# Kernel optimization log

Measured on AMD Instinct MI355X. Metric: run time of the kernel, lower is better.

## Reference

```python
import jax, jax.numpy as jnp
import numpy as np

N_NODES = 100000
N_EDGES = 1600000
N_GRAPHS = 64
IN_DIM, HID, OUT_DIM = 64, 128, 32


def _glorot(key, shape):
    lim = float(np.sqrt(6.0 / (shape[0] + shape[1])))
    return jax.random.uniform(key, shape, jnp.float32, -lim, lim)


def setup_inputs() -> dict:
    key = jax.random.key(0)
    ks = jax.random.split(key, 20)
    x = jax.random.normal(ks[0], (N_NODES, IN_DIM), jnp.float32)
    edge_index = jax.random.randint(ks[1], (2, N_EDGES), 0, N_NODES, jnp.int64)
    batch = jnp.sort(jax.random.randint(ks[2], (N_NODES,), 0, N_GRAPHS, jnp.int64))
    d = {"x": x, "edge_index": edge_index, "batch": batch}
    dims = [(IN_DIM, HID), (HID, HID), (HID, HID), (HID, HID), (HID, OUT_DIM)]
    names = ["W1", "W2", "W3", "W4", "Wo"]
    bnames = ["b1", "b2", "b3", "b4", "bo"]
    for i, ((di, do), wn, bn) in enumerate(zip(dims, names, bnames)):
        d[wn] = _glorot(ks[3 + i], (di, do))
        d[bn] = jnp.zeros((do,), jnp.float32)
    # MLP: 32 -> 64 -> 8 -> 8  (hidden_dim//2, output_dim//2, output_dim//4)
    mdims = [(OUT_DIM, HID // 2), (HID // 2, OUT_DIM // 2), (OUT_DIM // 2, OUT_DIM // 4)]
    for i, (di, do) in enumerate(mdims):
        d[f"M{i+1}w"] = _glorot(ks[10 + i], (di, do))
        d[f"M{i+1}b"] = jnp.zeros((do,), jnp.float32)
    return d


def _gcn(x, src, dst, norm, W, b, n):
    h = x @ W                                    # [N, d_out] dense GEMM
    msg = h[src] * norm[:, None]                 # gather + normalize
    agg = jax.ops.segment_sum(msg, dst, num_segments=n)  # scatter-add
    return agg + b


def reference(x, edge_index, batch, W1, b1, W2, b2, W3, b3, W4, b4, Wo, bo,
              M1w, M1b, M2w, M2b, M3w, M3b):
    n = x.shape[0]
    # add self loops (PyG GCNConv default)
    loops = jnp.arange(n, dtype=edge_index.dtype)
    src = jnp.concatenate([edge_index[0], loops])
    dst = jnp.concatenate([edge_index[1], loops])
    # symmetric degree normalization: D^{-1/2} (A+I) D^{-1/2}
    deg = jax.ops.segment_sum(jnp.ones_like(src, dtype=x.dtype), dst, num_segments=n)
    dinv = jnp.where(deg > 0, jax.lax.rsqrt(deg), 0.0)
    norm = dinv[src] * dinv[dst]                 # [E+N]

    h = jax.nn.relu(_gcn(x, src, dst, norm, W1, b1, n))
    for W, b in ((W2, b2), (W3, b3), (W4, b4)):
        h = jax.nn.relu(_gcn(h, src, dst, norm, W, b, n))
    h = _gcn(h, src, dst, norm, Wo, bo, n)       # [N, 32]

    # global mean pool over graphs
    sums = jax.ops.segment_sum(h, batch, num_segments=N_GRAPHS)
    cnts = jax.ops.segment_sum(jnp.ones((n,), h.dtype), batch, num_segments=N_GRAPHS)
    g = sums / jnp.maximum(cnts, 1.0)[:, None]   # [G, 32]

    g = jax.nn.relu(g @ M1w + M1b)
    g = jax.nn.relu(g @ M2w + M2b)
    return g @ M3w + M3b                          # [G, 8]
```

## Files before the change

kernel.cpp:

```cpp
#include <hip/hip_runtime.h>


static constexpr int TPB = 256;
static constexpr int NBKT = 128;
static constexpr int NCHK = 256;

using f32x4  = __attribute__((ext_vector_type(4))) float;
using bf16x8 = __attribute__((ext_vector_type(8))) short;

__device__ __forceinline__ float u2f(unsigned u) { return __uint_as_float(u); }

__device__ __forceinline__ unsigned short bf1(float a) {
    unsigned u = __float_as_uint(a);
    u += 0x7FFFu + ((u >> 16) & 1u);
    return (unsigned short)(u >> 16);
}

__device__ __forceinline__ unsigned bf2(float a, float b) {
    unsigned ua = __float_as_uint(a);
    unsigned ub = __float_as_uint(b);
    ua += 0x7FFFu + ((ua >> 16) & 1u);
    ub += 0x7FFFu + ((ub >> 16) & 1u);
    return (ua >> 16) | (ub & 0xFFFF0000u);
}

__global__ __launch_bounds__(256) void k_hist(const int* __restrict__ dst,
                                              int* __restrict__ histT, int E, int CS) {
    __shared__ int h[NBKT];
    int c = blockIdx.x, t = threadIdx.x;
    if (t < NBKT) h[t] = 0;
    __syncthreads();
    int e0 = c * CS, e1 = min(e0 + CS, E);
    for (int e = e0 + t; e < e1; e += 256)
        atomicAdd(&h[dst[e] >> 10], 1);
    __syncthreads();
    if (t < NBKT) histT[t * NCHK + c] = h[t];
}

__global__ __launch_bounds__(256) void k_scanS(const int* __restrict__ histT,
                                               int* __restrict__ stg) {
    constexpr int TOT = NBKT * NCHK;
    constexpr int PER = TOT / 256;
    __shared__ int s[256];
    int t = threadIdx.x;
    int base = t * PER;
    int sum = 0;
    for (int i = 0; i < PER; ++i) sum += histT[base + i];
    s[t] = sum;
    __syncthreads();
    for (int off = 1; off < 256; off <<= 1) {
        int add = (t >= off) ? s[t - off] : 0;
        __syncthreads();
        s[t] += add;
        __syncthreads();
    }
    int run = (t > 0) ? s[t - 1] : 0;
    for (int i = 0; i < PER; ++i) {
        stg[base + i] = run;
        run += histT[base + i];
    }
}

__global__ __launch_bounds__(256) void k_bucket(const int* __restrict__ src,
                                                const int* __restrict__ dst,
                                                const int* __restrict__ stg,
                                                unsigned* __restrict__ staging,
                                                int E, int CS) {
    __shared__ int cur[NBKT];
    int c = blockIdx.x, t = threadIdx.x;
    if (t < NBKT) cur[t] = stg[t * NCHK + c];
    __syncthreads();
    int e0 = c * CS, e1 = min(e0 + CS, E);
    for (int e = e0 + t; e < e1; e += 256) {
        int d = dst[e];
        int p = atomicAdd(&cur[d >> 10], 1);
        staging[p] = ((unsigned)src[e] << 10) | (unsigned)(d & 1023);
    }
}

__global__ __launch_bounds__(256) void k_deg(const unsigned* __restrict__ staging,
                                             const int* __restrict__ stg,
                                             int* __restrict__ cnt, int E, int n) {
    __shared__ int deg[1024];
    int r = blockIdx.x, t = threadIdx.x;
    for (int i = t; i < 1024; i += 256) deg[i] = 0;
    __syncthreads();
    int s0 = stg[r * NCHK];
    int s1 = (r == NBKT - 1) ? E : stg[(r + 1) * NCHK];
    for (int e = s0 + t; e < s1; e += 256)
        atomicAdd(&deg[staging[e] & 1023u], 1);
    __syncthreads();
    int b = r << 10;
    for (int i = t; i < 1024; i += 256)
        if (b + i < n) cnt[b + i] = deg[i];
}

__global__ void k_scanA(const int* __restrict__ cnt, int* __restrict__ rowptr,
                        int* __restrict__ bsum, int n) {
    __shared__ int s[TPB];
    int t = threadIdx.x;
    int i = blockIdx.x * TPB + t;
    s[t] = (i < n) ? cnt[i] : 0;
    __syncthreads();
    for (int off = 1; off < TPB; off <<= 1) {
        int add = (t >= off) ? s[t - off] : 0;
        __syncthreads();
        s[t] += add;
        __syncthreads();
    }
    if (i < n) rowptr[i + 1] = s[t];
    if (t == TPB - 1) bsum[blockIdx.x] = s[t];
}

__global__ void k_scanB(const int* __restrict__ bsum, int* __restrict__ bscan, int nb) {
    __shared__ int s[512];
    int t = threadIdx.x;
    s[t] = (t < nb) ? bsum[t] : 0;
    __syncthreads();
    for (int off = 1; off < 512; off <<= 1) {
        int add = (t >= off) ? s[t - off] : 0;
        __syncthreads();
        s[t] += add;
        __syncthreads();
    }
    if (t < nb) bscan[t] = (t > 0) ? s[t - 1] : 0;
}

__global__ void k_scanC(int* __restrict__ rowptr, const int* __restrict__ bscan,
                        const int* __restrict__ cnt, float* __restrict__ dinv, int n) {
    int i = blockIdx.x * blockDim.x + threadIdx.x;
    if (i >= n) return;
    rowptr[i + 1] += bscan[i >> 8];
    dinv[i] = rsqrtf((float)cnt[i] + 1.0f);
    if (i == 0) rowptr[0] = 0;
}

__global__ __launch_bounds__(256) void k_fill2(const unsigned* __restrict__ staging,
                                               const int* __restrict__ stg,
                                               const int* __restrict__ rowptr,
                                               int* __restrict__ csr, int E, int n) {
    __shared__ int cur[1024];
    int r = blockIdx.x, t = threadIdx.x;
    int b = r << 10;
    for (int i = t; i < 1024; i += 256)
        cur[i] = (b + i < n) ? rowptr[b + i] : 0;
    __syncthreads();
    int s0 = stg[r * NCHK];
    int s1 = (r == NBKT - 1) ? E : stg[(r + 1) * NCHK];
    for (int e = s0 + t; e < s1; e += 256) {
        unsigned sd = staging[e];
        int p = atomicAdd(&cur[sd & 1023u], 1);
        csr[p] = (int)(sd >> 10);
    }
}

__global__ void k_castx(const float* __restrict__ x, const float* __restrict__ dinv,
                        unsigned short* __restrict__ xs, int n) {
    int gid = blockIdx.x * blockDim.x + threadIdx.x;
    if (gid >= n * 8) return;
    int row = gid >> 3;
    float d = dinv[row];
    const float4* xp = (const float4*)x + (size_t)gid * 2;
    float4 a = xp[0], b = xp[1];
    uint4 o;
    o.x = bf2(a.x * d, a.y * d);
    o.y = bf2(a.z * d, a.w * d);
    o.z = bf2(b.x * d, b.y * d);
    o.w = bf2(b.z * d, b.w * d);
    ((uint4*)xs)[gid] = o;
}

__global__ void k_prepw(const float* __restrict__ W1, const float* __restrict__ W2,
                        const float* __restrict__ W3, const float* __restrict__ W4,
                        const float* __restrict__ Wo,
                        unsigned short* __restrict__ wt1, unsigned short* __restrict__ wt2,
                        unsigned short* __restrict__ wt3, unsigned short* __restrict__ wt4,
                        unsigned short* __restrict__ wto) {
    int b = blockIdx.x, k = threadIdx.x;
    const float* W; unsigned short* wt; int K, OUT, nn;
    if (b < 128)      { W = W1; wt = wt1; K = 64;  OUT = 128; nn = b; }
    else if (b < 256) { W = W2; wt = wt2; K = 128; OUT = 128; nn = b - 128; }
    else if (b < 384) { W = W3; wt = wt3; K = 128; OUT = 128; nn = b - 256; }
    else if (b < 512) { W = W4; wt = wt4; K = 128; OUT = 128; nn = b - 384; }
    else              { W = Wo; wt = wto; K = 128; OUT = 32;  nn = b - 512; }
    if (nn >= OUT || k >= K) return;
    float v = W[(size_t)k * OUT + nn];
    unsigned short hi = bf1(v);
    float fhi = u2f((unsigned)hi << 16);
    unsigned short lo = bf1(v - fhi);
    wt[nn * K + k] = hi;
    wt[OUT * K + nn * K + k] = lo;
}

template <int K, int OUT, int EPI>
__global__ __launch_bounds__(256) void k_gemm_mfma(
    const unsigned short* __restrict__ Ain,
    const unsigned short* __restrict__ WT,
    const float* __restrict__ dinv,
    const float* __restrict__ bias,
    unsigned short* __restrict__ out, int n) {
    constexpr int NT = OUT / 16;
    constexpr int KT = K / 32;
    constexpr int CH = K / 8;
    __shared__ __align__(16) unsigned short Wl[2 * OUT * K];

    int t = threadIdx.x;
    {
        const uint4* wg = (const uint4*)WT;
        uint4* wl = (uint4*)Wl;
        for (int i = t; i < 2 * OUT * CH; i += 256) {
            int m = i / (OUT * CH);
            int r = i - m * (OUT * CH);
            int nn = r / CH, g = r - nn * CH;
            wl[m * OUT * CH + nn * CH + (g ^ (nn & 7))] = wg[i];
        }
    }

    int wid = t >> 6, lane = t & 63;
    int lr = lane & 15, lg = lane >> 4;
    int mbase = blockIdx.x * 128 + wid * 32;

    bf16x8 a[2][KT];
#pragma unroll
    for (int mt = 0; mt < 2; ++mt) {
        int row = mbase + mt * 16 + lr;
        row = row < n ? row : n - 1;
        const bf16x8* ap = (const bf16x8*)(Ain + (size_t)row * K);
#pragma unroll
        for (int kt = 0; kt < KT; ++kt)
            a[mt][kt] = ap[kt * 4 + lg];
    }

    __syncthreads();

    f32x4 acc[2][NT] = {};
#pragma unroll
    for (int nt = 0; nt < NT; ++nt) {
        int nn = nt * 16 + lr;
        int swz = nn & 7;
        int rowoff = nn * K;
#pragma unroll
        for (int kt = 0; kt < KT; ++kt) {
            int g = kt * 4 + lg;
            int off = rowoff + ((g ^ swz) * 8);
            bf16x8 bhi = *(const bf16x8*)&Wl[off];
            bf16x8 blo = *(const bf16x8*)&Wl[OUT * K + off];
#pragma unroll
            for (int mt = 0; mt < 2; ++mt) {
                acc[mt][nt] = __builtin_amdgcn_mfma_f32_16x16x32_bf16(
                    a[mt][kt], bhi, acc[mt][nt], 0, 0, 0);
                acc[mt][nt] = __builtin_amdgcn_mfma_f32_16x16x32_bf16(
                    a[mt][kt], blo, acc[mt][nt], 0, 0, 0);
            }
        }
    }

#pragma unroll
    for (int mt = 0; mt < 2; ++mt) {
        int rbase = mbase + mt * 16 + lg * 4;
        float dv[4];
        if (EPI == 0) {
#pragma unroll
            for (int r = 0; r < 4; ++r)
                dv[r] = (rbase + r < n) ? dinv[rbase + r] : 0.f;
        }
#pragma unroll
        for (int nt = 0; nt < NT; ++nt) {
            int col = nt * 16 + lr;
            float bb = (EPI == 1) ? bias[col] : 0.f;
#pragma unroll
            for (int r = 0; r < 4; ++r) {
                int row = rbase + r;
                if (row < n) {
                    float v = acc[mt][nt][r];
                    if (EPI == 0) v *= dv[r];
                    else v = fmaxf(v + bb, 0.f);
                    out[(size_t)row * OUT + col] = bf1(v);
                }
            }
        }
    }
}

__device__ __forceinline__ void addbf(float* acc, uint4 w) {
    acc[0] += u2f(w.x << 16); acc[1] += u2f(w.x & 0xFFFF0000u);
    acc[2] += u2f(w.y << 16); acc[3] += u2f(w.y & 0xFFFF0000u);
    acc[4] += u2f(w.z << 16); acc[5] += u2f(w.z & 0xFFFF0000u);
    acc[6] += u2f(w.w << 16); acc[7] += u2f(w.w & 0xFFFF0000u);
}

template <int D, bool RELU, bool HASBIAS, bool OUTBF>
__global__ __launch_bounds__(256) void k_gather_bf(const unsigned short* __restrict__ hsb,
                                                   const int* __restrict__ rowptr,
                                                   const int* __restrict__ csr,
                                                   const float* __restrict__ dinv,
                                                   const float* __restrict__ bias,
                                                   void* __restrict__ outp, int n) {
    constexpr int TPN = D / 8;
    int gid = blockIdx.x * blockDim.x + threadIdx.x;
    int node = gid / TPN;
    if (node >= n) return;
    int c = gid % TPN;
    const uint4* hb = (const uint4*)hsb;

    float acc[8];
    {
        uint4 v = hb[(size_t)node * TPN + c];
        acc[0] = u2f(v.x << 16); acc[1] = u2f(v.x & 0xFFFF0000u);
        acc[2] = u2f(v.y << 16); acc[3] = u2f(v.y & 0xFFFF0000u);
        acc[4] = u2f(v.z << 16); acc[5] = u2f(v.z & 0xFFFF0000u);
        acc[6] = u2f(v.w << 16); acc[7] = u2f(v.w & 0xFFFF0000u);
    }
    int j0 = rowptr[node], j1 = rowptr[node + 1];
    int j = j0;
    for (; j + 3 < j1; j += 4) {
        int s0 = csr[j], s1 = csr[j + 1], s2 = csr[j + 2], s3 = csr[j + 3];
        uint4 w0 = hb[(size_t)s0 * TPN + c];
        uint4 w1 = hb[(size_t)s1 * TPN + c];
        uint4 w2 = hb[(size_t)s2 * TPN + c];
        uint4 w3 = hb[(size_t)s3 * TPN + c];
        addbf(acc, w0); addbf(acc, w1); addbf(acc, w2); addbf(acc, w3);
    }
    for (; j < j1; ++j) {
        uint4 w0 = hb[(size_t)csr[j] * TPN + c];
        addbf(acc, w0);
    }

    float di = dinv[node];
    float r[8];
    if (HASBIAS) {
        float4 b0 = *(const float4*)&bias[c * 8];
        float4 b1 = *(const float4*)&bias[c * 8 + 4];
        r[0] = di * acc[0] + b0.x; r[1] = di * acc[1] + b0.y;
        r[2] = di * acc[2] + b0.z; r[3] = di * acc[3] + b0.w;
        r[4] = di * acc[4] + b1.x; r[5] = di * acc[5] + b1.y;
        r[6] = di * acc[6] + b1.z; r[7] = di * acc[7] + b1.w;
    } else {
#pragma unroll
        for (int i = 0; i < 8; ++i) r[i] = di * acc[i];
    }
    if (RELU) {
#pragma unroll
        for (int i = 0; i < 8; ++i) r[i] = fmaxf(r[i], 0.f);
    }
    if (OUTBF) {
        uint4 o;
        o.x = bf2(r[0], r[1]); o.y = bf2(r[2], r[3]);
        o.z = bf2(r[4], r[5]); o.w = bf2(r[6], r[7]);
        ((uint4*)outp)[(size_t)node * TPN + c] = o;
    } else {
        float4 o0 = {r[0], r[1], r[2], r[3]};
        float4 o1 = {r[4], r[5], r[6], r[7]};
        float4* op = (float4*)outp + (size_t)node * TPN * 2 + c * 2;
        op[0] = o0;
        op[1] = o1;
    }
}

__global__ __launch_bounds__(256) void k_pool(const float* __restrict__ h,
                                              const int* __restrict__ batch,
                                              float* __restrict__ g, int n) {
    __shared__ int se[2];
    __shared__ float red[8][32];
    int gi = blockIdx.x;
    int t = threadIdx.x;
    if (t == 0) {
        int lo = 0, hi = n;
        while (lo < hi) { int m = (lo + hi) >> 1; if (batch[m] < gi) lo = m + 1; else hi = m; }
        se[0] = lo;
        lo = 0; hi = n;
        while (lo < hi) { int m = (lo + hi) >> 1; if (batch[m] < gi + 1) lo = m + 1; else hi = m; }
        se[1] = lo;
    }
    __syncthreads();
    int start = se[0], end = se[1];
    int col = t & 31, sub = t >> 5;
    float acc = 0.f;
    for (int i = start + sub; i < end; i += 8)
        acc += h[(size_t)i * 32 + col];
    red[sub][col] = acc;
    __syncthreads();
    if (t < 32) {
        float s = 0.f;
#pragma unroll
        for (int q = 0; q < 8; ++q) s += red[q][t];
        float c = (float)(end - start);
        g[gi * 32 + t] = s / fmaxf(c, 1.0f);
    }
}

template <int K, int O, bool RELU>
__global__ void k_mlp(const float* __restrict__ in, const float* __restrict__ W,
                      const float* __restrict__ b, float* __restrict__ out, int G) {
    int gid = blockIdx.x * blockDim.x + threadIdx.x;
    if (gid >= G * O) return;
    int g = gid / O, j = gid % O;
    float s = b[j];
    for (int k = 0; k < K; ++k) s += in[g * K + k] * W[k * O + j];
    if (RELU) s = fmaxf(s, 0.f);
    out[gid] = s;
}

extern "C" void kernel_launch(void* const* d_in, const int* in_sizes, int n_in,
                              void* d_out, int out_size, void* d_ws, size_t ws_size,
                              hipStream_t stream) {
    const float* x    = (const float*)d_in[0];
    const int*   ei   = (const int*)d_in[1];
    const int*   batch= (const int*)d_in[2];
    const float* W1 = (const float*)d_in[3];  const float* b1 = (const float*)d_in[4];
    const float* W2 = (const float*)d_in[5];  const float* b2 = (const float*)d_in[6];
    const float* W3 = (const float*)d_in[7];  const float* b3 = (const float*)d_in[8];
    const float* W4 = (const float*)d_in[9];  const float* b4 = (const float*)d_in[10];
    const float* Wo = (const float*)d_in[11]; const float* bo = (const float*)d_in[12];
    const float* M1w = (const float*)d_in[13]; const float* M1b = (const float*)d_in[14];
    const float* M2w = (const float*)d_in[15]; const float* M2b = (const float*)d_in[16];
    const float* M3w = (const float*)d_in[17]; const float* M3b = (const float*)d_in[18];

    const int N = in_sizes[0] / 64;
    const int E = in_sizes[1] / 2;
    const int G = out_size / 8;
    const int* src  = ei;
    const int* dstp = ei + E;

    char* w = (char*)d_ws;
    unsigned short* buf1 = (unsigned short*)w; w += (size_t)N * 128 * 2;
    unsigned short* buf2 = (unsigned short*)w; w += (size_t)N * 128 * 2;
    unsigned short* hsb  = (unsigned short*)w; w += (size_t)N * 128 * 2;
    int*      csr     = (int*)w;      w += (size_t)E * 4;
    unsigned* staging = (unsigned*)w; w += (size_t)E * 4;
    int*      histT   = (int*)w;      w += NBKT * NCHK * 4;
    int*      stg     = (int*)w;      w += NBKT * NCHK * 4;
    int*      cnt     = (int*)w;      w += (size_t)N * 4;
    int*      rowptr  = (int*)w;      w += (size_t)(N + 4) * 4;
    int*      bsum    = (int*)w;      w += 4096;
    int*      bscan   = (int*)w;      w += 4096;
    float*    dinv    = (float*)w;    w += (size_t)N * 4;
    unsigned short* wt1 = (unsigned short*)w; w += 2 * 128 * 64 * 2;
    unsigned short* wt2 = (unsigned short*)w; w += 2 * 128 * 128 * 2;
    unsigned short* wt3 = (unsigned short*)w; w += 2 * 128 * 128 * 2;
    unsigned short* wt4 = (unsigned short*)w; w += 2 * 128 * 128 * 2;
    unsigned short* wto = (unsigned short*)w; w += 2 * 32 * 128 * 2;
    float*    gp      = (float*)w;    w += 64 * 32 * 4;
    float*    m1      = (float*)w;    w += 64 * 64 * 4;
    float*    m2      = (float*)w;    w += 64 * 16 * 4;

    const int NB = (N + TPB - 1) / TPB;
    const int CS = (E + NCHK - 1) / NCHK;
    const int GB = (N + 127) / 128;

    k_hist<<<NCHK, 256, 0, stream>>>(dstp, histT, E, CS);
    k_prepw<<<544, 128, 0, stream>>>(W1, W2, W3, W4, Wo, wt1, wt2, wt3, wt4, wto);
    k_scanS<<<1, 256, 0, stream>>>(histT, stg);
    k_bucket<<<NCHK, 256, 0, stream>>>(src, dstp, stg, staging, E, CS);
    k_deg<<<NBKT, 256, 0, stream>>>(staging, stg, cnt, E, N);
    k_scanA<<<NB, TPB, 0, stream>>>(cnt, rowptr, bsum, N);
    k_scanB<<<1, 512, 0, stream>>>(bsum, bscan, NB);
    k_scanC<<<NB, TPB, 0, stream>>>(rowptr, bscan, cnt, dinv, N);
    k_fill2<<<NBKT, 256, 0, stream>>>(staging, stg, rowptr, csr, E, N);

    unsigned short* agg = buf1;
    unsigned short* xs  = buf2;

    k_castx<<<(N * 8 + 255) / 256, 256, 0, stream>>>(x, dinv, xs, N);
    k_gather_bf<64, false, false, true><<<(N * 8 + 255) / 256, 256, 0, stream>>>(
        xs, rowptr, csr, dinv, nullptr, agg, N);
    k_gemm_mfma<64, 128, 1><<<GB, 256, 0, stream>>>(agg, wt1, nullptr, b1, buf2, N);

    k_gemm_mfma<128, 128, 0><<<GB, 256, 0, stream>>>(buf2, wt2, dinv, nullptr, hsb, N);
    k_gather_bf<128, true, true, true><<<(N * 16 + 255) / 256, 256, 0, stream>>>(
        hsb, rowptr, csr, dinv, b2, buf1, N);
    k_gemm_mfma<128, 128, 0><<<GB, 256, 0, stream>>>(buf1, wt3, dinv, nullptr, hsb, N);
    k_gather_bf<128, true, true, true><<<(N * 16 + 255) / 256, 256, 0, stream>>>(
        hsb, rowptr, csr, dinv, b3, buf2, N);
    k_gemm_mfma<128, 128, 0><<<GB, 256, 0, stream>>>(buf2, wt4, dinv, nullptr, hsb, N);
    k_gather_bf<128, true, true, true><<<(N * 16 + 255) / 256, 256, 0, stream>>>(
        hsb, rowptr, csr, dinv, b4, buf1, N);

    k_gemm_mfma<128, 32, 0><<<GB, 256, 0, stream>>>(buf1, wto, dinv, nullptr, hsb, N);
    float* hout = (float*)buf2;
    k_gather_bf<32, false, true, false><<<(N * 4 + 255) / 256, 256, 0, stream>>>(
        hsb, rowptr, csr, dinv, bo, hout, N);

    k_pool<<<G, 256, 0, stream>>>(hout, batch, gp, N);
    k_mlp<32, 64, true><<<(G * 64 + 255) / 256, 256, 0, stream>>>(gp, M1w, M1b, m1, G);
    k_mlp<64, 16, true><<<(G * 16 + 255) / 256, 256, 0, stream>>>(m1, M2w, M2b, m2, G);
    k_mlp<16, 8, false><<<(G * 8 + 255) / 256, 256, 0, stream>>>(m2, M3w, M3b, (float*)d_out, G);
}
```

Measured before the change: 626.4 us.

## Split gather into column slices per block and use nontemporal index/output accesses

The gather kernel now assigns each block 128 nodes and a 16-column slice, with two threads per node and consecutive blocks sweeping slices of the same nodes. Each block touches a narrower column range of the feature matrix, which is meant to improve cache locality for the random neighbor gathers. CSR index loads, rowptr loads and output stores use nontemporal hints so streaming data does not evict the reused features from cache. The trade-off is that rowptr and csr are now re-read once per slice.

```diff
diff --git a/kernel.cpp b/kernel.cpp
--- a/kernel.cpp
+++ b/kernel.cpp
@@ -6,6 +6,7 @@
 static constexpr int NCHK = 256;
 
 using f32x4  = __attribute__((ext_vector_type(4))) float;
+using u32x4  = __attribute__((ext_vector_type(4))) unsigned;
 using bf16x8 = __attribute__((ext_vector_type(8))) short;
 
 __device__ __forceinline__ float u2f(unsigned u) { return __uint_as_float(u); }
@@ -282,7 +283,7 @@
     }
 }
 
-__device__ __forceinline__ void addbf(float* acc, uint4 w) {
+__device__ __forceinline__ void addbf(float* acc, u32x4 w) {
     acc[0] += u2f(w.x << 16); acc[1] += u2f(w.x & 0xFFFF0000u);
     acc[2] += u2f(w.y << 16); acc[3] += u2f(w.y & 0xFFFF0000u);
     acc[4] += u2f(w.z << 16); acc[5] += u2f(w.z & 0xFFFF0000u);
@@ -290,47 +291,54 @@
 }
 
 template <int D, bool RELU, bool HASBIAS, bool OUTBF>
-__global__ __launch_bounds__(256) void k_gather_bf(const unsigned short* __restrict__ hsb,
-                                                   const int* __restrict__ rowptr,
-                                                   const int* __restrict__ csr,
-                                                   const float* __restrict__ dinv,
-                                                   const float* __restrict__ bias,
-                                                   void* __restrict__ outp, int n) {
-    constexpr int TPN = D / 8;
-    int gid = blockIdx.x * blockDim.x + threadIdx.x;
-    int node = gid / TPN;
+__global__ __launch_bounds__(256) void k_gather_sl(
+    const unsigned short* __restrict__ hsb,
+    const int* __restrict__ rowptr, const int* __restrict__ csr,
+    const float* __restrict__ dinv, const float* __restrict__ bias,
+    void* __restrict__ outp, int n) {
+    constexpr int NSL = D / 16;
+    constexpr int RW = D / 8;
+    int slice = blockIdx.x % NSL;
+    int nb = blockIdx.x / NSL;
+    int t = threadIdx.x;
+    int node = nb * 128 + (t >> 1);
     if (node >= n) return;
-    int c = gid % TPN;
-    const uint4* hb = (const uint4*)hsb;
+    int cidx = slice * 2 + (t & 1);
+    const u32x4* hb = (const u32x4*)hsb;
 
     float acc[8];
     {
-        uint4 v = hb[(size_t)node * TPN + c];
+        u32x4 v = hb[(size_t)node * RW + cidx];
         acc[0] = u2f(v.x << 16); acc[1] = u2f(v.x & 0xFFFF0000u);
         acc[2] = u2f(v.y << 16); acc[3] = u2f(v.y & 0xFFFF0000u);
         acc[4] = u2f(v.z << 16); acc[5] = u2f(v.z & 0xFFFF0000u);
         acc[6] = u2f(v.w << 16); acc[7] = u2f(v.w & 0xFFFF0000u);
     }
-    int j0 = rowptr[node], j1 = rowptr[node + 1];
+    int j0 = __builtin_nontemporal_load(&rowptr[node]);
+    int j1 = __builtin_nontemporal_load(&rowptr[node + 1]);
     int j = j0;
     for (; j + 3 < j1; j += 4) {
-        int s0 = csr[j], s1 = csr[j + 1], s2 = csr[j + 2], s3 = csr[j + 3];
-        uint4 w0 = hb[(size_t)s0 * TPN + c];
-        uint4 w1 = hb[(size_t)s1 * TPN + c];
-        uint4 w2 = hb[(size_t)s2 * TPN + c];
-        uint4 w3 = hb[(size_t)s3 * TPN + c];
+        int s0 = __builtin_nontemporal_load(&csr[j]);
+        int s1 = __builtin_nontemporal_load(&csr[j + 1]);
+        int s2 = __builtin_nontemporal_load(&csr[j + 2]);
+        int s3 = __builtin_nontemporal_load(&csr[j + 3]);
+        u32x4 w0 = hb[(size_t)s0 * RW + cidx];
+        u32x4 w1 = hb[(size_t)s1 * RW + cidx];
+        u32x4 w2 = hb[(size_t)s2 * RW + cidx];
+        u32x4 w3 = hb[(size_t)s3 * RW + cidx];
         addbf(acc, w0); addbf(acc, w1); addbf(acc, w2); addbf(acc, w3);
     }
     for (; j < j1; ++j) {
-        uint4 w0 = hb[(size_t)csr[j] * TPN + c];
+        int s0 = __builtin_nontemporal_load(&csr[j]);
+        u32x4 w0 = hb[(size_t)s0 * RW + cidx];
         addbf(acc, w0);
     }
 
     float di = dinv[node];
     float r[8];
     if (HASBIAS) {
-        float4 b0 = *(const float4*)&bias[c * 8];
-        float4 b1 = *(const float4*)&bias[c * 8 + 4];
+        float4 b0 = *(const float4*)&bias[cidx * 8];
+        float4 b1 = *(const float4*)&bias[cidx * 8 + 4];
         r[0] = di * acc[0] + b0.x; r[1] = di * acc[1] + b0.y;
         r[2] = di * acc[2] + b0.z; r[3] = di * acc[3] + b0.w;
         r[4] = di * acc[4] + b1.x; r[5] = di * acc[5] + b1.y;
@@ -344,16 +352,16 @@
         for (int i = 0; i < 8; ++i) r[i] = fmaxf(r[i], 0.f);
     }
     if (OUTBF) {
-        uint4 o;
+        u32x4 o;
         o.x = bf2(r[0], r[1]); o.y = bf2(r[2], r[3]);
         o.z = bf2(r[4], r[5]); o.w = bf2(r[6], r[7]);
-        ((uint4*)outp)[(size_t)node * TPN + c] = o;
+        __builtin_nontemporal_store(o, &((u32x4*)outp)[(size_t)node * RW + cidx]);
     } else {
-        float4 o0 = {r[0], r[1], r[2], r[3]};
-        float4 o1 = {r[4], r[5], r[6], r[7]};
-        float4* op = (float4*)outp + (size_t)node * TPN * 2 + c * 2;
-        op[0] = o0;
-        op[1] = o1;
+        f32x4 o0 = {r[0], r[1], r[2], r[3]};
+        f32x4 o1 = {r[4], r[5], r[6], r[7]};
+        f32x4* op = (f32x4*)outp + (size_t)node * (D / 4) + cidx * 2;
+        __builtin_nontemporal_store(o0, op);
+        __builtin_nontemporal_store(o1, op + 1);
     }
 }
 
@@ -447,6 +455,7 @@
     const int NB = (N + TPB - 1) / TPB;
     const int CS = (E + NCHK - 1) / NCHK;
     const int GB = (N + 127) / 128;
+    const int SB = (N + 127) / 128;
 
     k_hist<<<NCHK, 256, 0, stream>>>(dstp, histT, E, CS);
     k_prepw<<<544, 128, 0, stream>>>(W1, W2, W3, W4, Wo, wt1, wt2, wt3, wt4, wto);
@@ -462,23 +471,23 @@
     unsigned short* xs  = buf2;
 
     k_castx<<<(N * 8 + 255) / 256, 256, 0, stream>>>(x, dinv, xs, N);
-    k_gather_bf<64, false, false, true><<<(N * 8 + 255) / 256, 256, 0, stream>>>(
+    k_gather_sl<64, false, false, true><<<4 * SB, 256, 0, stream>>>(
         xs, rowptr, csr, dinv, nullptr, agg, N);
     k_gemm_mfma<64, 128, 1><<<GB, 256, 0, stream>>>(agg, wt1, nullptr, b1, buf2, N);
 
     k_gemm_mfma<128, 128, 0><<<GB, 256, 0, stream>>>(buf2, wt2, dinv, nullptr, hsb, N);
-    k_gather_bf<128, true, true, true><<<(N * 16 + 255) / 256, 256, 0, stream>>>(
+    k_gather_sl<128, true, true, true><<<8 * SB, 256, 0, stream>>>(
         hsb, rowptr, csr, dinv, b2, buf1, N);
     k_gemm_mfma<128, 128, 0><<<GB, 256, 0, stream>>>(buf1, wt3, dinv, nullptr, hsb, N);
-    k_gather_bf<128, true, true, true><<<(N * 16 + 255) / 256, 256, 0, stream>>>(
+    k_gather_sl<128, true, true, true><<<8 * SB, 256, 0, stream>>>(
         hsb, rowptr, csr, dinv, b3, buf2, N);
     k_gemm_mfma<128, 128, 0><<<GB, 256, 0, stream>>>(buf2, wt4, dinv, nullptr, hsb, N);
-    k_gather_bf<128, true, true, true><<<(N * 16 + 255) / 256, 256, 0, stream>>>(
+    k_gather_sl<128, true, true, true><<<8 * SB, 256, 0, stream>>>(
         hsb, rowptr, csr, dinv, b4, buf1, N);
 
     k_gemm_mfma<128, 32, 0><<<GB, 256, 0, stream>>>(buf1, wto, dinv, nullptr, hsb, N);
     float* hout = (float*)buf2;
-    k_gather_bf<32, false, true, false><<<(N * 4 + 255) / 256, 256, 0, stream>>>(
+    k_gather_sl<32, false, true, false><<<2 * SB, 256, 0, stream>>>(
         hsb, rowptr, csr, dinv, bo, hout, N);
 
     k_pool<<<G, 256, 0, stream>>>(hout, batch, gp, N);
```

New measurement: 1.289 ms. 106% more time.

## Stage bucket scatter in LDS tiles for coalesced staging writes

Applied to the files above, without the earlier changes.

The edge-bucketing kernel now handles edges in 2048-element tiles. Each tile gets a local counting sort by destination bucket in shared memory, with per-bucket counts and a prefix scan, and is then written to the global staging array in bucket-contiguous runs. Before, each edge was written to a scattered global address. The aim is coalesced global writes and fewer global atomics, at the cost of more barriers and extra shared-memory traffic. The buf2 workspace size is also doubled, which looks incidental.

```diff
diff --git a/kernel.cpp b/kernel.cpp
--- a/kernel.cpp
+++ b/kernel.cpp
@@ -4,6 +4,7 @@
 static constexpr int TPB = 256;
 static constexpr int NBKT = 128;
 static constexpr int NCHK = 256;
+static constexpr int TILE = 2048;
 
 using f32x4  = __attribute__((ext_vector_type(4))) float;
 using bf16x8 = __attribute__((ext_vector_type(8))) short;
@@ -66,15 +67,59 @@
                                                 const int* __restrict__ stg,
                                                 unsigned* __restrict__ staging,
                                                 int E, int CS) {
-    __shared__ int cur[NBKT];
+    __shared__ int gcur[NBKT];
+    __shared__ int cnt_[NBKT];
+    __shared__ int base[NBKT];
+    __shared__ unsigned sval[TILE];
+    __shared__ unsigned char sbkt[TILE];
     int c = blockIdx.x, t = threadIdx.x;
-    if (t < NBKT) cur[t] = stg[t * NCHK + c];
-    __syncthreads();
+    if (t < NBKT) gcur[t] = stg[t * NCHK + c];
     int e0 = c * CS, e1 = min(e0 + CS, E);
-    for (int e = e0 + t; e < e1; e += 256) {
-        int d = dst[e];
-        int p = atomicAdd(&cur[d >> 10], 1);
-        staging[p] = ((unsigned)src[e] << 10) | (unsigned)(d & 1023);
+
+    for (int tb = e0; tb < e1; tb += TILE) {
+        int m = min(TILE, e1 - tb);
+        __syncthreads();
+        if (t < NBKT) cnt_[t] = 0;
+        __syncthreads();
+        int  b_[8]; unsigned v_[8]; int o_[8]; bool ok_[8];
+#pragma unroll
+        for (int k = 0; k < 8; ++k) {
+            int e = tb + t + k * 256;
+            ok_[k] = (e < tb + m);
+            b_[k] = 0; v_[k] = 0; o_[k] = 0;
+            if (ok_[k]) {
+                int d = dst[e];
+                b_[k] = d >> 10;
+                v_[k] = ((unsigned)src[e] << 10) | (unsigned)(d & 1023);
+                o_[k] = atomicAdd(&cnt_[b_[k]], 1);
+            }
+        }
+        __syncthreads();
+        if (t < NBKT) base[t] = cnt_[t];
+        __syncthreads();
+        for (int off = 1; off < NBKT; off <<= 1) {
+            int v = (t < NBKT && t >= off) ? base[t - off] : 0;
+            __syncthreads();
+            if (t < NBKT) base[t] += v;
+            __syncthreads();
+        }
+        if (t < NBKT) base[t] -= cnt_[t];
+        __syncthreads();
+#pragma unroll
+        for (int k = 0; k < 8; ++k) {
+            if (ok_[k]) {
+                int p = base[b_[k]] + o_[k];
+                sval[p] = v_[k];
+                sbkt[p] = (unsigned char)b_[k];
+            }
+        }
+        __syncthreads();
+        for (int i = t; i < m; i += 256) {
+            int b = sbkt[i];
+            staging[gcur[b] + (i - base[b])] = sval[i];
+        }
+        __syncthreads();
+        if (t < NBKT) gcur[t] += cnt_[t];
     }
 }
 
@@ -424,7 +469,7 @@
 
     char* w = (char*)d_ws;
     unsigned short* buf1 = (unsigned short*)w; w += (size_t)N * 128 * 2;
-    unsigned short* buf2 = (unsigned short*)w; w += (size_t)N * 128 * 2;
+    unsigned short* buf2 = (unsigned short*)w; w += (size_t)N * 128 * 4;
     unsigned short* hsb  = (unsigned short*)w; w += (size_t)N * 128 * 2;
     int*      csr     = (int*)w;      w += (size_t)E * 4;
     unsigned* staging = (unsigned*)w; w += (size_t)E * 4;
```

New measurement: 628.8 us. Within noise of the previous version (+0.4%).
